# Kernel tuning notes

Hardware: AMD Instinct MI355X
Metric: run time of the kernel (lower is better)

## Reference

```python
import jax, jax.numpy as jnp
import numpy as np
from jax import lax

B, H, W, C = 4, 96, 96, 256
F = 256
KH = KW = 3
K = KH * KW
DG = 1
CG = C // DG
SH = SW = 1
DH = DW = 1
PAD_T = (DH * (KH - 1)) // 2  # 'same' padding (top/left) for 3x3 dil 1
PAD_L = (DW * (KW - 1)) // 2


def setup_inputs() -> dict:
    key = jax.random.key(0)
    k1, k2, k3 = jax.random.split(key, 3)
    x = jax.random.normal(k1, (B, H, W, C), jnp.float32)
    # offset/mask conv weights (orig init zeros; small random to exercise sampling)
    om_kernel = jax.random.normal(k2, (KH, KW, C, DG * 3 * K), jnp.float32) * 0.01
    om_bias = jnp.zeros((DG * 3 * K,), jnp.float32)
    stdv = 1.0 / np.sqrt(C * KH * KW)
    kernel = jax.random.uniform(k3, (K * C, F), jnp.float32, -stdv, stdv)
    bias = jnp.zeros((F,), jnp.float32)
    return {"x": x, "om_kernel": om_kernel, "om_bias": om_bias, "kernel": kernel, "bias": bias}


def reference(x, om_kernel, om_bias, kernel, bias):
    Bx, Hx, Wx, Cx = x.shape
    # offset/mask prediction conv (NHWC, 'SAME', matches keras Conv2D)
    om = lax.conv_general_dilated(
        x, om_kernel, (SH, SW), "SAME", rhs_dilation=(DH, DW),
        dimension_numbers=("NHWC", "HWIO", "NHWC")) + om_bias
    Ho, Wo = om.shape[1], om.shape[2]
    off = om[..., : 2 * DG * K].reshape(Bx, Ho, Wo, DG, K, 2)  # (dy, dx) per group/kpoint
    mask = jax.nn.sigmoid(om[..., 2 * DG * K :]).reshape(Bx, Ho, Wo, DG, K) * 2.0

    # base sampling grid: y = ho*SH - PAD_T + ki*DH (+ dy), similarly x
    base_y = (jnp.arange(Ho) * SH - PAD_T)[:, None] + (jnp.arange(KH) * DH)[None, :]  # [Ho,KH]
    base_x = (jnp.arange(Wo) * SW - PAD_L)[:, None] + (jnp.arange(KW) * DW)[None, :]  # [Wo,KW]
    gy = jnp.broadcast_to(base_y[:, None, :, None], (Ho, Wo, KH, KW)).reshape(Ho, Wo, K)
    gx = jnp.broadcast_to(base_x[None, :, None, :], (Ho, Wo, KH, KW)).reshape(Ho, Wo, K)

    py = gy[None, :, :, None, :].astype(x.dtype) + off[..., 0]  # [B,Ho,Wo,DG,K]
    px = gx[None, :, :, None, :].astype(x.dtype) + off[..., 1]

    # reorder to [B, N, DG] with N = Ho*Wo*K (K varies fastest after spatial)
    N = Ho * Wo * K
    py = py.transpose(0, 1, 2, 4, 3).reshape(Bx, N, DG)
    px = px.transpose(0, 1, 2, 4, 3).reshape(Bx, N, DG)
    mask_t = mask.transpose(0, 1, 2, 4, 3).reshape(Bx, N, DG)

    y0 = jnp.floor(py)
    x0 = jnp.floor(px)
    fy = py - y0
    fx = px - x0

    xf = x.reshape(Bx, Hx * Wx, DG, CG)
    val = jnp.zeros((Bx, N, DG, CG), x.dtype)
    for yi, wy in ((y0, 1.0 - fy), (y0 + 1.0, fy)):
        for xi, wx in ((x0, 1.0 - fx), (x0 + 1.0, fx)):
            valid = (yi >= 0) & (yi < Hx) & (xi >= 0) & (xi < Wx)
            yc = jnp.clip(yi, 0, Hx - 1).astype(jnp.int32)
            xc = jnp.clip(xi, 0, Wx - 1).astype(jnp.int32)
            lin = yc * Wx + xc  # [B,N,DG]
            g = jnp.take_along_axis(xf, lin[..., None], axis=1)  # [B,N,DG,CG]
            val = val + g * (wy * wx * valid.astype(x.dtype))[..., None]

    # modulate and im2col -> GEMM
    cols = (val * mask_t[..., None]).reshape(Bx, Ho * Wo, K * Cx)
    out = jnp.matmul(cols, kernel).reshape(Bx, Ho, Wo, -1) + bias
    return out
```

## Files before the change

kernel.cpp:

```cpp
#include <hip/hip_runtime.h>
#include <hip/hip_bf16.h>
#include <stdint.h>
#include <stddef.h>


namespace {
constexpr int H  = 96, W = 96, C = 256, F = 256;
constexpr int HP = 98;
constexpr int NP = 4 * 96 * 96;
constexpr int KC = 9 * 256;

constexpr int NB_PAD  = 4 * HP * HP / 8;
constexpr int NB_OMW  = 9 * 32;
constexpr int NB_WT   = (KC / 64) * (F / 64);
constexpr int NB_ZERO = NP * 32 * 4 / 4096;
}

typedef __attribute__((ext_vector_type(8))) short bf16x8;
typedef __attribute__((ext_vector_type(4))) float floatx4;

__device__ __forceinline__ void load_lds16(const void* g, void* l) {
  __builtin_amdgcn_global_load_lds((const __attribute__((address_space(1))) void*)g,
                                   (__attribute__((address_space(3))) void*)l,
                                   16, 0, 0);
}

__device__ __forceinline__ uint32_t pk2(float lo, float hi) {
  __hip_bfloat162 t = __float22bfloat162_rn(float2{lo, hi});
  return *reinterpret_cast<uint32_t*>(&t);
}

__device__ __forceinline__ void acc8(uint4 v, float w, float* a) {
  a[0] += w * __uint_as_float(v.x << 16); a[1] += w * __uint_as_float(v.x & 0xffff0000u);
  a[2] += w * __uint_as_float(v.y << 16); a[3] += w * __uint_as_float(v.y & 0xffff0000u);
  a[4] += w * __uint_as_float(v.z << 16); a[5] += w * __uint_as_float(v.z & 0xffff0000u);
  a[6] += w * __uint_as_float(v.w << 16); a[7] += w * __uint_as_float(v.w & 0xffff0000u);
}

__global__ __launch_bounds__(256) void k_prep(const float* __restrict__ x,
                                              const float* __restrict__ omk,
                                              const float* __restrict__ kern,
                                              uint4* __restrict__ xp4,
                                              __hip_bfloat16* __restrict__ wom,
                                              __hip_bfloat16* __restrict__ wt,
                                              float4* __restrict__ pOmz) {
  __shared__ float t[64][65];
  const int bi = blockIdx.x, tid = threadIdx.x;

  if (bi < NB_PAD) {
    const int sub = tid >> 5, cid = tid & 31;
    const int pp  = bi * 8 + sub;
    const int b   = pp / (HP * HP);
    const int r   = pp % (HP * HP);
    const int y   = r / HP, xq = r % HP;
    uint4 o = {0u, 0u, 0u, 0u};
    if (y >= 1 && y <= H && xq >= 1 && xq <= W) {
      const float* src = x + ((size_t)((b * H + (y - 1)) * W + (xq - 1))) * C + cid * 8;
      const float4 v0 = *(const float4*)src;
      const float4 v1 = *(const float4*)(src + 4);
      o.x = pk2(v0.x, v0.y); o.y = pk2(v0.z, v0.w);
      o.z = pk2(v1.x, v1.y); o.w = pk2(v1.z, v1.w);
    }
    xp4[(size_t)pp * 32 + cid] = o;
  } else if (bi < NB_PAD + NB_OMW) {
    const int i  = bi - NB_PAD;
    const int kk = i / 32, oc = i % 32;
    float v = (oc < 27) ? omk[(size_t)(kk * 256 + tid) * 27 + oc] : 0.f;
    wom[(size_t)oc * KC + kk * 256 + tid] = __float2bfloat16(v);
  } else if (bi < NB_PAD + NB_OMW + NB_WT) {
    const int j   = bi - NB_PAD - NB_OMW;
    const int kc0 = (j % (KC / 64)) * 64, f0 = (j / (KC / 64)) * 64;
    const int rr = tid >> 6, cc = tid & 63;
#pragma unroll
    for (int i = 0; i < 16; ++i)
      t[rr * 16 + i][cc] = kern[(size_t)(kc0 + rr * 16 + i) * F + f0 + cc];
    __syncthreads();
#pragma unroll
    for (int i = 0; i < 16; ++i) {
      const int frow = rr * 16 + i;
      wt[(size_t)(f0 + frow) * KC + kc0 + cc] = __float2bfloat16(t[cc][frow]);
    }
  } else {
    const int j = bi - NB_PAD - NB_OMW - NB_WT;
    pOmz[(size_t)j * 256 + tid] = (float4){0.f, 0.f, 0.f, 0.f};
  }
}

__global__ __launch_bounds__(256) void k_omgemm(const __hip_bfloat16* __restrict__ xp,
                                                const __hip_bfloat16* __restrict__ wom,
                                                float* __restrict__ pOm) {
  __shared__ __align__(16) char lds[20480];
  const int tid  = threadIdx.x;
  const int xr   = blockIdx.x;
  const int xs   = (xr & 7) * 36 + (xr >> 3);
  const int m0   = xs * 128;
  const int s    = blockIdx.y;
  const int lane = tid & 63, wave = tid >> 6;
  const int quad = lane >> 4, l16 = lane & 15;

  const int kp = (tid & 3) ^ ((tid >> 3) & 3);
  const __hip_bfloat16* abase[2];
#pragma unroll
  for (int j = 0; j < 2; ++j) {
    const int row = (tid >> 2) + j * 64;
    const int p = m0 + row;
    const int b = p / (H * W);
    const int hw = p % (H * W);
    const int h = hw / W, w = hw % W;
    abase[j] = xp + ((size_t)(b * HP + h) * HP + w) * C + kp * 8;
  }
  const __hip_bfloat16* bbase = wom + (size_t)(tid >> 2) * KC + kp * 8;

  auto stage = [&](int buf, int k0) {
    const int kk = k0 >> 8, c0 = k0 & 255;
    const int aoff = ((kk / 3) * HP + (kk % 3)) * C + c0;
    char* base = &lds[buf * 10240];
    load_lds16(abase[0] + aoff, base + tid * 16);
    load_lds16(abase[1] + aoff, base + 4096 + tid * 16);
    if (tid < 128) load_lds16(bbase + k0, base + 8192 + tid * 16);
  };

  floatx4 acc[2][2];
#pragma unroll
  for (int i = 0; i < 2; ++i)
#pragma unroll
    for (int j = 0; j < 2; ++j) acc[i][j] = (floatx4){0.f, 0.f, 0.f, 0.f};

  const int swq = (quad ^ ((l16 >> 1) & 3)) * 16;

  const int kbeg = s * 384, kend = kbeg + 384;
  stage(0, kbeg);
  int cur = 0;
#pragma unroll 1
  for (int k0 = kbeg; k0 < kend; k0 += 32) {
    __syncthreads();
    if (k0 + 32 < kend) stage(cur ^ 1, k0 + 32);
    const char* base = &lds[cur * 10240];

    bf16x8 af[2], bfr[2];
#pragma unroll
    for (int mt = 0; mt < 2; ++mt)
      af[mt] = *(const bf16x8*)&base[(wave * 32 + mt * 16 + l16) * 64 + swq];
#pragma unroll
    for (int nt = 0; nt < 2; ++nt)
      bfr[nt] = *(const bf16x8*)&base[8192 + (nt * 16 + l16) * 64 + swq];
#pragma unroll
    for (int mt = 0; mt < 2; ++mt)
#pragma unroll
      for (int nt = 0; nt < 2; ++nt)
        acc[mt][nt] = __builtin_amdgcn_mfma_f32_16x16x32_bf16(af[mt], bfr[nt], acc[mt][nt], 0, 0, 0);
    cur ^= 1;
  }

#pragma unroll
  for (int mt = 0; mt < 2; ++mt)
#pragma unroll
    for (int nt = 0; nt < 2; ++nt) {
      const int gm = m0 + wave * 32 + mt * 16 + quad * 4;
      const int gn = nt * 16 + l16;
#pragma unroll
      for (int r = 0; r < 4; ++r)
        __hip_atomic_fetch_add(&pOm[(size_t)(gm + r) * 32 + gn], acc[mt][nt][r],
                               __ATOMIC_RELAXED, __HIP_MEMORY_SCOPE_AGENT);
    }
}

__global__ __launch_bounds__(256) void k_sample(const uint4* __restrict__ xp4,
                                                const float* __restrict__ pOm,
                                                const float* __restrict__ om_bias,
                                                uint4* __restrict__ cols4) {
  __shared__ float2 s_ow[8][9][4];

  const int tid = threadIdx.x;
  const int sub = tid >> 5, cid = tid & 31;
  const int bs  = (blockIdx.x & 7) * 576 + (blockIdx.x >> 3);

  if (tid < 72) {
    const int ps = tid / 9, k = tid % 9;
    const int p  = bs * 8 + ps;
    const int b  = p / (H * W);
    const int hw = p % (H * W);
    const int h = hw / W, w = hw % W;
    const float dy = om_bias[2 * k]     + pOm[(size_t)p * 32 + 2 * k];
    const float dx = om_bias[2 * k + 1] + pOm[(size_t)p * 32 + 2 * k + 1];
    const float mv = om_bias[18 + k]    + pOm[(size_t)p * 32 + 18 + k];
    const float m  = 2.f / (1.f + __expf(-mv));
    const float sy = (float)(h - 1 + k / 3) + dy;
    const float sx = (float)(w - 1 + k % 3) + dx;
    const float y0f = floorf(sy), x0f = floorf(sx);
    const float fy = sy - y0f, fx = sx - x0f;
    const int y0 = (int)y0f, x0 = (int)x0f;
#pragma unroll
    for (int c2 = 0; c2 < 4; ++c2) {
      const int dy2 = c2 >> 1, dx2 = c2 & 1;
      const int yi = y0 + dy2, xi = x0 + dx2;
      const bool valid = (yi >= 0) & (yi < H) & (xi >= 0) & (xi < W);
      const float wgt = valid ? (dy2 ? fy : 1.f - fy) * (dx2 ? fx : 1.f - fx) * m : 0.f;
      const int yc = min(max(yi + 1, 0), HP - 1);
      const int xc = min(max(xi + 1, 0), HP - 1);
      const int off = ((b * HP + yc) * HP + xc) * 32;
      s_ow[ps][k][c2] = float2{__int_as_float(off), wgt};
    }
  }
  __syncthreads();

  const int p = bs * 8 + sub;
  uint4* __restrict__ ob = cols4 + (size_t)p * 288 + cid;

#pragma unroll 1
  for (int k = 0; k < 9; ++k) {
    const float2 ow0 = s_ow[sub][k][0], ow1 = s_ow[sub][k][1];
    const float2 ow2 = s_ow[sub][k][2], ow3 = s_ow[sub][k][3];
    float a[8] = {0.f, 0.f, 0.f, 0.f, 0.f, 0.f, 0.f, 0.f};
    acc8(xp4[(size_t)__float_as_int(ow0.x) + cid], ow0.y, a);
    acc8(xp4[(size_t)__float_as_int(ow1.x) + cid], ow1.y, a);
    acc8(xp4[(size_t)__float_as_int(ow2.x) + cid], ow2.y, a);
    acc8(xp4[(size_t)__float_as_int(ow3.x) + cid], ow3.y, a);
    uint4 o;
    o.x = pk2(a[0], a[1]); o.y = pk2(a[2], a[3]);
    o.z = pk2(a[4], a[5]); o.w = pk2(a[6], a[7]);
    ob[k * 32] = o;
  }
}

__global__ __launch_bounds__(256) void k_gemm(const __hip_bfloat16* __restrict__ A,
                                              const __hip_bfloat16* __restrict__ Bt,
                                              const float* __restrict__ bias,
                                              float* __restrict__ out) {
  __shared__ __align__(16) char lds[28672];

  const int tid  = threadIdx.x;
  const int m0   = blockIdx.x * 96;
  const int n0   = blockIdx.y * 128;
  const int lane = tid & 63, wave = tid >> 6;
  const int wm = wave & 1, wn = wave >> 1;
  const int quad = lane >> 4, l16 = lane & 15;

  const int row = tid >> 2, kp = (tid & 3) ^ ((tid >> 3) & 3);
  const __hip_bfloat16* a0 = A  + (size_t)(m0 + row) * KC + kp * 8;
  const __hip_bfloat16* a1 = A  + (size_t)(m0 + 64 + row) * KC + kp * 8;
  const __hip_bfloat16* b0 = Bt + (size_t)(n0 + row) * KC + kp * 8;
  const __hip_bfloat16* b1 = Bt + (size_t)(n0 + 64 + row) * KC + kp * 8;

  auto stage = [&](int buf, int k0) {
    char* base = &lds[buf * 14336];
    load_lds16(a0 + k0, base + tid * 16);
    if (tid < 128) load_lds16(a1 + k0, base + 4096 + tid * 16);
    load_lds16(b0 + k0, base + 6144 + tid * 16);
    load_lds16(b1 + k0, base + 10240 + tid * 16);
  };

  floatx4 acc[3][4];
#pragma unroll
  for (int i = 0; i < 3; ++i)
#pragma unroll
    for (int j = 0; j < 4; ++j) acc[i][j] = (floatx4){0.f, 0.f, 0.f, 0.f};

  const int swq = (quad ^ ((l16 >> 1) & 3)) * 16;

  stage(0, 0);
  int cur = 0;
#pragma unroll 1
  for (int k0 = 0; k0 < KC; k0 += 32) {
    __syncthreads();
    if (k0 + 32 < KC) stage(cur ^ 1, k0 + 32);
    const char* base = &lds[cur * 14336];

    bf16x8 af[3], bfr[4];
#pragma unroll
    for (int mt = 0; mt < 3; ++mt)
      af[mt] = *(const bf16x8*)&base[(wm * 48 + mt * 16 + l16) * 64 + swq];
#pragma unroll
    for (int nt = 0; nt < 4; ++nt)
      bfr[nt] = *(const bf16x8*)&base[6144 + (wn * 64 + nt * 16 + l16) * 64 + swq];
#pragma unroll
    for (int mt = 0; mt < 3; ++mt)
#pragma unroll
      for (int nt = 0; nt < 4; ++nt)
        acc[mt][nt] = __builtin_amdgcn_mfma_f32_16x16x32_bf16(af[mt], bfr[nt], acc[mt][nt], 0, 0, 0);
    cur ^= 1;
  }

#pragma unroll
  for (int mt = 0; mt < 3; ++mt) {
#pragma unroll
    for (int nt = 0; nt < 4; ++nt) {
      const int gm = m0 + wm * 48 + mt * 16 + quad * 4;
      const int gn = n0 + wn * 64 + nt * 16 + l16;
      const float bs = bias[gn];
#pragma unroll
      for (int r = 0; r < 4; ++r)
        out[(size_t)(gm + r) * F + gn] = acc[mt][nt][r] + bs;
    }
  }
}

extern "C" void kernel_launch(void* const* d_in, const int* in_sizes, int n_in,
                              void* d_out, int out_size, void* d_ws, size_t ws_size,
                              hipStream_t stream) {
  const float* x    = (const float*)d_in[0];
  const float* omk  = (const float*)d_in[1];
  const float* omb  = (const float*)d_in[2];
  const float* kern = (const float*)d_in[3];
  const float* bias = (const float*)d_in[4];
  float* out = (float*)d_out;

  char* ws = (char*)d_ws;
  size_t off = 0;
  __hip_bfloat16* wt   = (__hip_bfloat16*)(ws + off); off += (size_t)F * KC * 2;
  __hip_bfloat16* xp   = (__hip_bfloat16*)(ws + off); off += (size_t)4 * HP * HP * C * 2;
  __hip_bfloat16* wom  = (__hip_bfloat16*)(ws + off); off += (size_t)32 * KC * 2;
  float*          pOm  = (float*)(ws + off);          off += (size_t)NP * 32 * 4;
  __hip_bfloat16* cols = (__hip_bfloat16*)(ws + off);

  k_prep  <<<dim3(NB_PAD + NB_OMW + NB_WT + NB_ZERO), 256, 0, stream>>>(
      x, omk, kern, (uint4*)xp, wom, wt, (float4*)pOm);
  k_omgemm<<<dim3(NP / 128, 6),      256, 0, stream>>>(xp, wom, pOm);
  k_sample<<<dim3(NP / 8),           256, 0, stream>>>((const uint4*)xp, pOm, omb, (uint4*)cols);
  k_gemm  <<<dim3(NP / 96, F / 128), 256, 0, stream>>>(cols, wt, bias, out);
}
```

Measured before the change: 222.0 us.

## Enlarge GEMM tile to 128x128 and use triple-buffered LDS pipeline

The main GEMM kernel grows its block tile from 96x128 to 128x128, so each wave computes 4x4 MFMA tiles. The double-buffered loop becomes a three-stage LDS ring: loads for two steps ahead are issued, and a partial vmcnt wait replaces a full drain before each barrier. The goal is more reuse per tile and better overlap of global-to-LDS loads with MFMA work. The cost is more LDS per block and more accumulator registers, which may lower occupancy, and fewer blocks (288 instead of 384) on a GPU with many CUs.

```diff
diff --git a/kernel.cpp b/kernel.cpp
--- a/kernel.cpp
+++ b/kernel.cpp
@@ -227,65 +227,77 @@
                                               const __hip_bfloat16* __restrict__ Bt,
                                               const float* __restrict__ bias,
                                               float* __restrict__ out) {
-  __shared__ __align__(16) char lds[28672];
+  __shared__ __align__(16) char lds[49152];
 
   const int tid  = threadIdx.x;
-  const int m0   = blockIdx.x * 96;
+  const int m0   = blockIdx.x * 128;
   const int n0   = blockIdx.y * 128;
   const int lane = tid & 63, wave = tid >> 6;
-  const int wm = wave & 1, wn = wave >> 1;
+  const int wm = wave >> 1, wn = wave & 1;
   const int quad = lane >> 4, l16 = lane & 15;
 
   const int row = tid >> 2, kp = (tid & 3) ^ ((tid >> 3) & 3);
   const __hip_bfloat16* a0 = A  + (size_t)(m0 + row) * KC + kp * 8;
-  const __hip_bfloat16* a1 = A  + (size_t)(m0 + 64 + row) * KC + kp * 8;
+  const __hip_bfloat16* a1 = a0 + (size_t)64 * KC;
   const __hip_bfloat16* b0 = Bt + (size_t)(n0 + row) * KC + kp * 8;
-  const __hip_bfloat16* b1 = Bt + (size_t)(n0 + 64 + row) * KC + kp * 8;
+  const __hip_bfloat16* b1 = b0 + (size_t)64 * KC;
 
   auto stage = [&](int buf, int k0) {
-    char* base = &lds[buf * 14336];
+    char* base = &lds[buf * 16384];
     load_lds16(a0 + k0, base + tid * 16);
-    if (tid < 128) load_lds16(a1 + k0, base + 4096 + tid * 16);
-    load_lds16(b0 + k0, base + 6144 + tid * 16);
-    load_lds16(b1 + k0, base + 10240 + tid * 16);
+    load_lds16(a1 + k0, base + 4096 + tid * 16);
+    load_lds16(b0 + k0, base + 8192 + tid * 16);
+    load_lds16(b1 + k0, base + 12288 + tid * 16);
   };
 
-  floatx4 acc[3][4];
-#pragma unroll
-  for (int i = 0; i < 3; ++i)
+  floatx4 acc[4][4];
+#pragma unroll
+  for (int i = 0; i < 4; ++i)
 #pragma unroll
     for (int j = 0; j < 4; ++j) acc[i][j] = (floatx4){0.f, 0.f, 0.f, 0.f};
 
   const int swq = (quad ^ ((l16 >> 1) & 3)) * 16;
 
+  auto compute = [&](const char* base) {
+    bf16x8 af[4], bfr[4];
+#pragma unroll
+    for (int mt = 0; mt < 4; ++mt)
+      af[mt] = *(const bf16x8*)&base[(wm * 64 + mt * 16 + l16) * 64 + swq];
+#pragma unroll
+    for (int nt = 0; nt < 4; ++nt)
+      bfr[nt] = *(const bf16x8*)&base[8192 + (wn * 64 + nt * 16 + l16) * 64 + swq];
+#pragma unroll
+    for (int mt = 0; mt < 4; ++mt)
+#pragma unroll
+      for (int nt = 0; nt < 4; ++nt)
+        acc[mt][nt] = __builtin_amdgcn_mfma_f32_16x16x32_bf16(af[mt], bfr[nt], acc[mt][nt], 0, 0, 0);
+  };
+
   stage(0, 0);
+  stage(1, 32);
   int cur = 0;
 #pragma unroll 1
-  for (int k0 = 0; k0 < KC; k0 += 32) {
-    __syncthreads();
-    if (k0 + 32 < KC) stage(cur ^ 1, k0 + 32);
-    const char* base = &lds[cur * 14336];
-
-    bf16x8 af[3], bfr[4];
-#pragma unroll
-    for (int mt = 0; mt < 3; ++mt)
-      af[mt] = *(const bf16x8*)&base[(wm * 48 + mt * 16 + l16) * 64 + swq];
-#pragma unroll
-    for (int nt = 0; nt < 4; ++nt)
-      bfr[nt] = *(const bf16x8*)&base[6144 + (wn * 64 + nt * 16 + l16) * 64 + swq];
-#pragma unroll
-    for (int mt = 0; mt < 3; ++mt)
-#pragma unroll
-      for (int nt = 0; nt < 4; ++nt)
-        acc[mt][nt] = __builtin_amdgcn_mfma_f32_16x16x32_bf16(af[mt], bfr[nt], acc[mt][nt], 0, 0, 0);
-    cur ^= 1;
-  }
-
-#pragma unroll
-  for (int mt = 0; mt < 3; ++mt) {
+  for (int t = 0; t < 70; ++t) {
+    asm volatile("s_waitcnt vmcnt(4)" ::: "memory");
+    __builtin_amdgcn_s_barrier();
+    int nb = cur + 2; if (nb >= 3) nb -= 3;
+    stage(nb, (t + 2) * 32);
+    compute(&lds[cur * 16384]);
+    cur = (cur == 2) ? 0 : cur + 1;
+  }
+  asm volatile("s_waitcnt vmcnt(4)" ::: "memory");
+  __builtin_amdgcn_s_barrier();
+  compute(&lds[cur * 16384]);
+  cur = (cur == 2) ? 0 : cur + 1;
+  asm volatile("s_waitcnt vmcnt(0)" ::: "memory");
+  __builtin_amdgcn_s_barrier();
+  compute(&lds[cur * 16384]);
+
+#pragma unroll
+  for (int mt = 0; mt < 4; ++mt) {
 #pragma unroll
     for (int nt = 0; nt < 4; ++nt) {
-      const int gm = m0 + wm * 48 + mt * 16 + quad * 4;
+      const int gm = m0 + wm * 64 + mt * 16 + quad * 4;
       const int gn = n0 + wn * 64 + nt * 16 + l16;
       const float bs = bias[gn];
 #pragma unroll
@@ -317,5 +329,5 @@
       x, omk, kern, (uint4*)xp, wom, wt, (float4*)pOm);
   k_omgemm<<<dim3(NP / 128, 6),      256, 0, stream>>>(xp, wom, pOm);
   k_sample<<<dim3(NP / 8),           256, 0, stream>>>((const uint4*)xp, pOm, omb, (uint4*)cols);
-  k_gemm  <<<dim3(NP / 96, F / 128), 256, 0, stream>>>(cols, wt, bias, out);
-}
+  k_gemm  <<<dim3(NP / 128, F / 128), 256, 0, stream>>>(cols, wt, bias, out);
+}
```

Result: slower. 241.5 us (+8.8%).

## Replace split-K atomic offset GEMM with full-K 64-row tiles and plain stores

Applied to the files above, without the earlier changes.

The offset/mask conv GEMM drops its 6-way split-K with atomic adds and instead gives each block a 64-row M tile over the full K range (576 blocks), writing results with plain stores. This removes the pOm zero-fill and the atomic traffic. The prep kernel is split into separate pad and weight-prep launches. In exchange each block runs a long serial K loop with less MFMA work per LDS stage, and the extra kernel launch adds overhead.

```diff
diff --git a/kernel.cpp b/kernel.cpp
--- a/kernel.cpp
+++ b/kernel.cpp
@@ -13,7 +13,6 @@
 constexpr int NB_PAD  = 4 * HP * HP / 8;
 constexpr int NB_OMW  = 9 * 32;
 constexpr int NB_WT   = (KC / 64) * (F / 64);
-constexpr int NB_ZERO = NP * 32 * 4 / 4096;
 }
 
 typedef __attribute__((ext_vector_type(8))) short bf16x8;
@@ -37,38 +36,38 @@
   a[6] += w * __uint_as_float(v.w << 16); a[7] += w * __uint_as_float(v.w & 0xffff0000u);
 }
 
-__global__ __launch_bounds__(256) void k_prep(const float* __restrict__ x,
-                                              const float* __restrict__ omk,
-                                              const float* __restrict__ kern,
-                                              uint4* __restrict__ xp4,
-                                              __hip_bfloat16* __restrict__ wom,
-                                              __hip_bfloat16* __restrict__ wt,
-                                              float4* __restrict__ pOmz) {
+__global__ __launch_bounds__(256) void k_pad(const float* __restrict__ x,
+                                             uint4* __restrict__ xp4) {
+  const int tid = threadIdx.x;
+  const int sub = tid >> 5, cid = tid & 31;
+  const int pp  = blockIdx.x * 8 + sub;
+  const int b   = pp / (HP * HP);
+  const int r   = pp % (HP * HP);
+  const int y   = r / HP, xq = r % HP;
+  uint4 o = {0u, 0u, 0u, 0u};
+  if (y >= 1 && y <= H && xq >= 1 && xq <= W) {
+    const float* src = x + ((size_t)((b * H + (y - 1)) * W + (xq - 1))) * C + cid * 8;
+    const float4 v0 = *(const float4*)src;
+    const float4 v1 = *(const float4*)(src + 4);
+    o.x = pk2(v0.x, v0.y); o.y = pk2(v0.z, v0.w);
+    o.z = pk2(v1.x, v1.y); o.w = pk2(v1.z, v1.w);
+  }
+  xp4[(size_t)pp * 32 + cid] = o;
+}
+
+__global__ __launch_bounds__(256) void k_wprep(const float* __restrict__ omk,
+                                               const float* __restrict__ kern,
+                                               __hip_bfloat16* __restrict__ wom,
+                                               __hip_bfloat16* __restrict__ wt) {
   __shared__ float t[64][65];
   const int bi = blockIdx.x, tid = threadIdx.x;
 
-  if (bi < NB_PAD) {
-    const int sub = tid >> 5, cid = tid & 31;
-    const int pp  = bi * 8 + sub;
-    const int b   = pp / (HP * HP);
-    const int r   = pp % (HP * HP);
-    const int y   = r / HP, xq = r % HP;
-    uint4 o = {0u, 0u, 0u, 0u};
-    if (y >= 1 && y <= H && xq >= 1 && xq <= W) {
-      const float* src = x + ((size_t)((b * H + (y - 1)) * W + (xq - 1))) * C + cid * 8;
-      const float4 v0 = *(const float4*)src;
-      const float4 v1 = *(const float4*)(src + 4);
-      o.x = pk2(v0.x, v0.y); o.y = pk2(v0.z, v0.w);
-      o.z = pk2(v1.x, v1.y); o.w = pk2(v1.z, v1.w);
-    }
-    xp4[(size_t)pp * 32 + cid] = o;
-  } else if (bi < NB_PAD + NB_OMW) {
-    const int i  = bi - NB_PAD;
-    const int kk = i / 32, oc = i % 32;
+  if (bi < NB_OMW) {
+    const int kk = bi / 32, oc = bi % 32;
     float v = (oc < 27) ? omk[(size_t)(kk * 256 + tid) * 27 + oc] : 0.f;
     wom[(size_t)oc * KC + kk * 256 + tid] = __float2bfloat16(v);
-  } else if (bi < NB_PAD + NB_OMW + NB_WT) {
-    const int j   = bi - NB_PAD - NB_OMW;
+  } else {
+    const int j   = bi - NB_OMW;
     const int kc0 = (j % (KC / 64)) * 64, f0 = (j / (KC / 64)) * 64;
     const int rr = tid >> 6, cc = tid & 63;
 #pragma unroll
@@ -80,89 +79,69 @@
       const int frow = rr * 16 + i;
       wt[(size_t)(f0 + frow) * KC + kc0 + cc] = __float2bfloat16(t[cc][frow]);
     }
-  } else {
-    const int j = bi - NB_PAD - NB_OMW - NB_WT;
-    pOmz[(size_t)j * 256 + tid] = (float4){0.f, 0.f, 0.f, 0.f};
   }
 }
 
 __global__ __launch_bounds__(256) void k_omgemm(const __hip_bfloat16* __restrict__ xp,
                                                 const __hip_bfloat16* __restrict__ wom,
                                                 float* __restrict__ pOm) {
-  __shared__ __align__(16) char lds[20480];
+  __shared__ __align__(16) char lds[12288];
   const int tid  = threadIdx.x;
   const int xr   = blockIdx.x;
-  const int xs   = (xr & 7) * 36 + (xr >> 3);
-  const int m0   = xs * 128;
-  const int s    = blockIdx.y;
+  const int xs   = (xr & 7) * 72 + (xr >> 3);
+  const int m0   = xs * 64;
   const int lane = tid & 63, wave = tid >> 6;
   const int quad = lane >> 4, l16 = lane & 15;
 
-  const int kp = (tid & 3) ^ ((tid >> 3) & 3);
-  const __hip_bfloat16* abase[2];
-#pragma unroll
-  for (int j = 0; j < 2; ++j) {
-    const int row = (tid >> 2) + j * 64;
-    const int p = m0 + row;
-    const int b = p / (H * W);
-    const int hw = p % (H * W);
-    const int h = hw / W, w = hw % W;
-    abase[j] = xp + ((size_t)(b * HP + h) * HP + w) * C + kp * 8;
-  }
-  const __hip_bfloat16* bbase = wom + (size_t)(tid >> 2) * KC + kp * 8;
+  const int kp  = (tid & 3) ^ ((tid >> 3) & 3);
+  const int row = tid >> 2;
+  {
+  }
+  const int p  = m0 + row;
+  const int b  = p / (H * W);
+  const int hw = p % (H * W);
+  const int h  = hw / W, w = hw % W;
+  const __hip_bfloat16* abase = xp + ((size_t)(b * HP + h) * HP + w) * C + kp * 8;
+  const __hip_bfloat16* bbase = wom + (size_t)row * KC + kp * 8;
 
   auto stage = [&](int buf, int k0) {
     const int kk = k0 >> 8, c0 = k0 & 255;
     const int aoff = ((kk / 3) * HP + (kk % 3)) * C + c0;
-    char* base = &lds[buf * 10240];
-    load_lds16(abase[0] + aoff, base + tid * 16);
-    load_lds16(abase[1] + aoff, base + 4096 + tid * 16);
-    if (tid < 128) load_lds16(bbase + k0, base + 8192 + tid * 16);
+    char* base = &lds[buf * 6144];
+    load_lds16(abase + aoff, base + tid * 16);
+    if (tid < 128) load_lds16(bbase + k0, base + 4096 + tid * 16);
   };
 
-  floatx4 acc[2][2];
-#pragma unroll
-  for (int i = 0; i < 2; ++i)
-#pragma unroll
-    for (int j = 0; j < 2; ++j) acc[i][j] = (floatx4){0.f, 0.f, 0.f, 0.f};
+  floatx4 acc[2];
+  acc[0] = (floatx4){0.f, 0.f, 0.f, 0.f};
+  acc[1] = (floatx4){0.f, 0.f, 0.f, 0.f};
 
   const int swq = (quad ^ ((l16 >> 1) & 3)) * 16;
 
-  const int kbeg = s * 384, kend = kbeg + 384;
-  stage(0, kbeg);
+  stage(0, 0);
   int cur = 0;
 #pragma unroll 1
-  for (int k0 = kbeg; k0 < kend; k0 += 32) {
+  for (int k0 = 0; k0 < KC; k0 += 32) {
     __syncthreads();
-    if (k0 + 32 < kend) stage(cur ^ 1, k0 + 32);
-    const char* base = &lds[cur * 10240];
-
-    bf16x8 af[2], bfr[2];
-#pragma unroll
-    for (int mt = 0; mt < 2; ++mt)
-      af[mt] = *(const bf16x8*)&base[(wave * 32 + mt * 16 + l16) * 64 + swq];
-#pragma unroll
-    for (int nt = 0; nt < 2; ++nt)
-      bfr[nt] = *(const bf16x8*)&base[8192 + (nt * 16 + l16) * 64 + swq];
-#pragma unroll
-    for (int mt = 0; mt < 2; ++mt)
-#pragma unroll
-      for (int nt = 0; nt < 2; ++nt)
-        acc[mt][nt] = __builtin_amdgcn_mfma_f32_16x16x32_bf16(af[mt], bfr[nt], acc[mt][nt], 0, 0, 0);
+    if (k0 + 32 < KC) stage(cur ^ 1, k0 + 32);
+    const char* base = &lds[cur * 6144];
+
+    bf16x8 af = *(const bf16x8*)&base[(wave * 16 + l16) * 64 + swq];
+    bf16x8 b0 = *(const bf16x8*)&base[4096 + (l16) * 64 + swq];
+    bf16x8 b1 = *(const bf16x8*)&base[4096 + (16 + l16) * 64 + swq];
+    acc[0] = __builtin_amdgcn_mfma_f32_16x16x32_bf16(af, b0, acc[0], 0, 0, 0);
+    acc[1] = __builtin_amdgcn_mfma_f32_16x16x32_bf16(af, b1, acc[1], 0, 0, 0);
     cur ^= 1;
   }
 
 #pragma unroll
-  for (int mt = 0; mt < 2; ++mt)
-#pragma unroll
-    for (int nt = 0; nt < 2; ++nt) {
-      const int gm = m0 + wave * 32 + mt * 16 + quad * 4;
-      const int gn = nt * 16 + l16;
-#pragma unroll
-      for (int r = 0; r < 4; ++r)
-        __hip_atomic_fetch_add(&pOm[(size_t)(gm + r) * 32 + gn], acc[mt][nt][r],
-                               __ATOMIC_RELAXED, __HIP_MEMORY_SCOPE_AGENT);
-    }
+  for (int nt = 0; nt < 2; ++nt) {
+    const int gm = m0 + wave * 16 + quad * 4;
+    const int gn = nt * 16 + l16;
+#pragma unroll
+    for (int r = 0; r < 4; ++r)
+      pOm[(size_t)(gm + r) * 32 + gn] = acc[nt][r];
+  }
 }
 
 __global__ __launch_bounds__(256) void k_sample(const uint4* __restrict__ xp4,
@@ -313,9 +292,9 @@
   float*          pOm  = (float*)(ws + off);          off += (size_t)NP * 32 * 4;
   __hip_bfloat16* cols = (__hip_bfloat16*)(ws + off);
 
-  k_prep  <<<dim3(NB_PAD + NB_OMW + NB_WT + NB_ZERO), 256, 0, stream>>>(
-      x, omk, kern, (uint4*)xp, wom, wt, (float4*)pOm);
-  k_omgemm<<<dim3(NP / 128, 6),      256, 0, stream>>>(xp, wom, pOm);
+  k_pad   <<<dim3(NB_PAD),           256, 0, stream>>>(x, (uint4*)xp);
+  k_wprep <<<dim3(NB_OMW + NB_WT),   256, 0, stream>>>(omk, kern, wom, wt);
+  k_omgemm<<<dim3(576),              256, 0, stream>>>(xp, wom, pOm);
   k_sample<<<dim3(NP / 8),           256, 0, stream>>>((const uint4*)xp, pOm, omb, (uint4*)cols);
   k_gemm  <<<dim3(NP / 96, F / 128), 256, 0, stream>>>(cols, wt, bias, out);
 }
```

Result: faster. 213.0 us (-4.1%).
